# Performance work log

Measured on AMD Instinct MI355X. Metric: run time of the kernel, lower is better.

Reference implementation:

```python
import jax, jax.numpy as jnp
import numpy as np

N_NODES = 30000
N_EDGES = 480000
N_GRAPHS = 128
CONV_PARAMS = [[32, 32], [32, 32], [64, 64], [64, 64], [128, 128], [128, 128]]
IN_FEAT = 5
NUM_CENTROID = 100
NUM_CLASS = 2
BN_EPS = 1e-5


def setup_inputs() -> dict:
    key = jax.random.key(0)
    ks = jax.random.split(key, 64)
    inp = {}
    inp['features'] = jax.random.normal(ks[0], (N_NODES, IN_FEAT), jnp.float32)
    inp['src'] = jax.random.randint(ks[1], (N_EDGES,), 0, N_NODES, jnp.int32)
    inp['dst'] = jax.random.randint(ks[2], (N_EDGES,), 0, N_NODES, jnp.int32)
    inp['graph_id'] = jnp.sort(jax.random.randint(ks[3], (N_NODES,), 0, N_GRAPHS, jnp.int32))
    inp['bn_gamma'] = jnp.ones((IN_FEAT,), jnp.float32)
    inp['bn_beta'] = jnp.zeros((IN_FEAT,), jnp.float32)
    in_f = IN_FEAT
    ki = 4
    for i, (c1, c2) in enumerate(CONV_PARAMS):
        # EdgeConv MLP operates on concat([x_i, x_j - x_i]) -> 2*in_f inputs
        s1 = 1.0 / np.sqrt(2 * in_f)
        s2 = 1.0 / np.sqrt(c1)
        inp[f'W1_{i}'] = jax.random.normal(ks[ki], (2 * in_f, c1), jnp.float32) * s1
        inp[f'b1_{i}'] = jnp.zeros((c1,), jnp.float32)
        inp[f'W2_{i}'] = jax.random.normal(ks[ki + 1], (c1, c2), jnp.float32) * s2
        inp[f'b2_{i}'] = jnp.zeros((c2,), jnp.float32)
        ki += 2
        in_f = c2
    inp['centroids'] = jax.random.normal(ks[ki], (NUM_CENTROID, CONV_PARAMS[-1][-1]), jnp.float32)
    inp['fc_w'] = jax.random.normal(ks[ki + 1], (NUM_CENTROID, NUM_CLASS), jnp.float32) * (1.0 / np.sqrt(NUM_CENTROID))
    inp['fc_b'] = jnp.zeros((NUM_CLASS,), jnp.float32)
    return inp


def _edge_conv(x, src, dst, deg_inv, W1, b1, W2, b2):
    # DGCNN-style EdgeConv: MLP([x_i, x_j - x_i]) then mean-aggregate to dst node
    xi = x[dst]                                   # [E, F]
    xj = x[src]                                   # [E, F]
    e = jnp.concatenate([xi, xj - xi], axis=-1)   # [E, 2F]
    h = jax.nn.relu(e @ W1 + b1)
    h = jax.nn.relu(h @ W2 + b2)
    return jax.ops.segment_sum(h, dst, num_segments=x.shape[0]) * deg_inv


def reference(features, src, dst, graph_id, bn_gamma, bn_beta,
              W1_0, b1_0, W2_0, b2_0, W1_1, b1_1, W2_1, b2_1,
              W1_2, b1_2, W2_2, b2_2, W1_3, b1_3, W2_3, b2_3,
              W1_4, b1_4, W2_4, b2_4, W1_5, b1_5, W2_5, b2_5,
              centroids, fc_w, fc_b):
    N = features.shape[0]
    # BatchNorm1d in training mode (batch statistics over nodes)
    mu = features.mean(axis=0)
    var = features.var(axis=0)
    x = (features - mu) / jnp.sqrt(var + BN_EPS) * bn_gamma + bn_beta

    # in-degree for mean aggregation
    deg = jax.ops.segment_sum(jnp.ones_like(dst, jnp.float32), dst, num_segments=N)
    deg_inv = (1.0 / jnp.maximum(deg, 1.0))[:, None]

    params = [(W1_0, b1_0, W2_0, b2_0), (W1_1, b1_1, W2_1, b2_1),
              (W1_2, b1_2, W2_2, b2_2), (W1_3, b1_3, W2_3, b2_3),
              (W1_4, b1_4, W2_4, b2_4), (W1_5, b1_5, W2_5, b2_5)]
    for W1, b1, W2, b2 in params:
        x = _edge_conv(x, src, dst, deg_inv, W1, b1, W2, b2)  # [N, c2]

    # CentroidDistance (Euclidean manifold): dist of each node to each centroid
    diff = x[:, None, :] - centroids[None, :, :]              # [N, C, D]
    dist = jnp.sqrt(jnp.sum(diff * diff, axis=-1) + 1e-12)    # [N, C]

    # per-graph mean pooling of centroid distances
    cnt = jax.ops.segment_sum(jnp.ones((N,), jnp.float32), graph_id, num_segments=N_GRAPHS)
    pooled = jax.ops.segment_sum(dist, graph_id, num_segments=N_GRAPHS) / jnp.maximum(cnt, 1.0)[:, None]

    return pooled @ fc_w + fc_b  # [G, num_class]
```

## Files before the change

kernel.cpp:

```cpp
#include <hip/hip_runtime.h>
#include <hip/hip_fp16.h>

#define N_NODES 30000
#define N_EDGES 480000
#define N_GRAPHS 128
#define IN_FEAT 5
#define NUM_CENTROID 100
#define BN_EPS 1e-5f

typedef unsigned int u32;
typedef unsigned short u16;

using half8 = __attribute__((ext_vector_type(8))) _Float16;
using h2    = __attribute__((ext_vector_type(2))) _Float16;
using f32x4 = __attribute__((ext_vector_type(4))) float;

__device__ __forceinline__ u16 f2h(float x) {
    return __half_as_ushort(__float2half_rn(x));
}
__device__ __forceinline__ float h2f(u16 h) {
    return __half2float(__ushort_as_half(h));
}
__device__ __forceinline__ u32 pack2h(float lo, float hi) {
    return (u32)f2h(lo) | ((u32)f2h(hi) << 16);
}

#define BN_BLKS 118
__global__ __launch_bounds__(256) void setup1_kernel(
    const float* __restrict__ f, float* __restrict__ acc,
    const int* __restrict__ dst, int* __restrict__ counts)
{
    __shared__ float s[10];
    const int b = blockIdx.x;
    if (b < BN_BLKS) {
        if (threadIdx.x < 10) s[threadIdx.x] = 0.f;
        __syncthreads();
        int n = b * 256 + threadIdx.x;
        if (n < N_NODES) {
            #pragma unroll
            for (int k = 0; k < IN_FEAT; ++k) {
                float v = f[n * IN_FEAT + k];
                atomicAdd(&s[k], v);
                atomicAdd(&s[5 + k], v * v);
            }
        }
        __syncthreads();
        if (threadIdx.x < 10) atomicAdd(&acc[threadIdx.x], s[threadIdx.x]);
    } else {
        int e = (b - BN_BLKS) * 256 + threadIdx.x;
        if (e < N_EDGES) atomicAdd(&counts[dst[e]], 1);
    }
}

__global__ __launch_bounds__(1024) void scan_kernel(
    const int* __restrict__ counts, int* __restrict__ row_off,
    float* __restrict__ deg_inv, int N)
{
    __shared__ int s[1024];
    const int CH = 30;
    int t = threadIdx.x;
    int base = t * CH;
    int loc = 0;
    for (int j = 0; j < CH; ++j) {
        int i = base + j;
        if (i < N) loc += counts[i];
    }
    s[t] = loc;
    __syncthreads();
    for (int off = 1; off < 1024; off <<= 1) {
        int v = (t >= off) ? s[t - off] : 0;
        __syncthreads();
        s[t] += v;
        __syncthreads();
    }
    int run = s[t] - loc;
    for (int j = 0; j < CH; ++j) {
        int i = base + j;
        if (i < N) {
            int cv = counts[i];
            row_off[i] = run;
            run += cv;
            deg_inv[i] = 1.0f / fmaxf((float)cv, 1.0f);
        }
    }
    if (t == 1023) row_off[N] = s[1023];
}

__constant__ __device__ const int LFIN[6] = {5, 32, 32, 64, 64, 128};
__constant__ __device__ const int LKD[6]  = {32, 32, 32, 64, 64, 128};
__constant__ __device__ const int LCD[6]  = {32, 32, 64, 64, 128, 128};
__constant__ __device__ const int W1OFF[6] = {0, 2048, 4096, 8192, 16384, 32768};
__constant__ __device__ const int W2OFF[6] = {0, 1024, 2048, 6144, 10240, 26624};
#define W1TOT 65536
#define W2TOT 43008
#define CTOT  14336
#define PREP_TOT (W1TOT + W2TOT + CTOT + 112)

#define CSR_BLKS 1875
#define BNN_BLKS 586

struct Setup2Args {
    const int* dst; const int* src; const int* row_off; int* cursor;
    int* csr_src; int* csr_dst;
    const float* f; const float* acc; const float* gamma; const float* beta;
    float* X0;
    const float* w1[6]; const float* w2[6]; const float* cent;
    u16* w1img; u16* w2img; u16* centimg; float* csq;
};

__global__ __launch_bounds__(256) void setup2_kernel(Setup2Args a)
{
    const int b = blockIdx.x;
    if (b < CSR_BLKS) {
        int e = b * 256 + threadIdx.x;
        if (e < N_EDGES) {
            int d = a.dst[e];
            int p = atomicAdd(&a.cursor[d], 1);
            a.csr_src[a.row_off[d] + p] = a.src[e];
            a.csr_dst[a.row_off[d] + p] = d;
        }
        return;
    }
    if (b < CSR_BLKS + BNN_BLKS) {
        int i = (b - CSR_BLKS) * 256 + threadIdx.x;
        if (i < N_NODES * IN_FEAT) {
            int k = i % IN_FEAT;
            float mu = a.acc[k] / (float)N_NODES;
            float var = a.acc[5 + k] / (float)N_NODES - mu * mu;
            float sc = a.gamma[k] / sqrtf(var + BN_EPS);
            a.X0[i] = (a.f[i] - mu) * sc + a.beta[k];
        }
        return;
    }
    int gid = (b - CSR_BLKS - BNN_BLKS) * 256 + threadIdx.x;
    if (gid < W1TOT) {
        int l = 0;
        #pragma unroll
        for (int i = 1; i < 6; ++i) if (gid >= W1OFF[i]) l = i;
        int local = gid - W1OFF[l];
        int K = LKD[l], C = LCD[l], F = LFIN[l];
        int n = local / K, k = local % K;
        float v = 0.f;
        if (k < F) {
            if (n < C) v = a.w1[l][k * C + n] - a.w1[l][(F + k) * C + n];
            else       v = a.w1[l][(F + k) * C + (n - C)];
        }
        int byte = (local * 2) ^ ((n & 7) << 4);
        *(u16*)((char*)a.w1img + (size_t)W1OFF[l] * 2 + byte) = f2h(v);
        return;
    }
    int g2 = gid - W1TOT;
    if (g2 < W2TOT) {
        int l = 0;
        #pragma unroll
        for (int i = 1; i < 6; ++i) if (g2 >= W2OFF[i]) l = i;
        int local = g2 - W2OFF[l];
        int C = LCD[l];
        int n = local / C, k = local % C;
        float v = a.w2[l][k * C + n];
        int byte = (local * 2) ^ ((n & 7) << 4);
        *(u16*)((char*)a.w2img + (size_t)W2OFF[l] * 2 + byte) = f2h(v);
        return;
    }
    int g3 = g2 - W2TOT;
    if (g3 < CTOT) {
        int c = g3 / 128, d = g3 % 128;
        float v = (c < NUM_CENTROID) ? a.cent[c * 128 + d] : 0.f;
        int byte = (g3 * 2) ^ ((c & 7) << 4);
        *(u16*)((char*)a.centimg + byte) = f2h(v);
        return;
    }
    int c = g3 - CTOT;
    if (c < 112) {
        float s = 0.f;
        if (c < NUM_CENTROID) {
            for (int d = 0; d < 128; ++d) {
                float cv = h2f(f2h(a.cent[c * 128 + d]));
                s += cv * cv;
            }
        }
        a.csq[c] = s;
    }
}

template <int FIN, int K, int C>
__global__ __launch_bounds__(256) void node_mfma_kernel(
    const float* __restrict__ Xin, const float* __restrict__ scale,
    const u16* __restrict__ w1img, const float* __restrict__ b1,
    u16* __restrict__ U, u16* __restrict__ V, int N)
{
    constexpr int COLS = 2 * C;
    __shared__ u16 wt[COLS * K];
    __shared__ u16 xt[32 * K];

    for (int i = threadIdx.x; i < COLS * K / 8; i += 256)
        reinterpret_cast<uint4*>(wt)[i] = reinterpret_cast<const uint4*>(w1img)[i];

    constexpr int DPT = K / 8;
    const int nl = threadIdx.x >> 3;
    const int part = threadIdx.x & 7;
    const int n = blockIdx.x * 32 + nl;
    const int k0 = part * DPT;
    const bool vld = (n < N);
    float s = 1.f;
    if (vld && scale) s = scale[n];

    float xv[DPT];
    if constexpr (FIN == K) {
        #pragma unroll
        for (int j4 = 0; j4 < DPT / 4; ++j4) {
            float4 f4 = {0, 0, 0, 0};
            if (vld) f4 = *reinterpret_cast<const float4*>(Xin + (size_t)n * FIN + k0 + j4 * 4);
            xv[j4 * 4 + 0] = f4.x * s; xv[j4 * 4 + 1] = f4.y * s;
            xv[j4 * 4 + 2] = f4.z * s; xv[j4 * 4 + 3] = f4.w * s;
        }
    } else {
        #pragma unroll
        for (int j = 0; j < DPT; ++j) {
            int k = k0 + j;
            xv[j] = (vld && k < FIN) ? Xin[(size_t)n * FIN + k] * s : 0.f;
        }
    }

    if constexpr (DPT == 4) {
        u32 o[2];
        o[0] = pack2h(xv[0], xv[1]);
        o[1] = pack2h(xv[2], xv[3]);
        int byte = ((nl * K + k0) * 2) ^ ((nl & 7) << 4);
        *reinterpret_cast<uint2*>((char*)xt + byte) = *reinterpret_cast<uint2*>(o);
    } else {
        #pragma unroll
        for (int j8 = 0; j8 < DPT / 8; ++j8) {
            u32 o[4];
            #pragma unroll
            for (int q = 0; q < 4; ++q)
                o[q] = pack2h(xv[j8 * 8 + q * 2], xv[j8 * 8 + q * 2 + 1]);
            int byte = ((nl * K + k0 + j8 * 8) * 2) ^ ((nl & 7) << 4);
            *reinterpret_cast<uint4*>((char*)xt + byte) = *reinterpret_cast<uint4*>(o);
        }
    }
    __syncthreads();

    constexpr int NT = COLS / 16;
    constexpr int NPW = NT / 4;
    constexpr int KS = K / 32;

    const int wid = threadIdx.x >> 6;
    const int lane = threadIdx.x & 63;
    const int lrow = lane & 15;
    const int lk8 = (lane >> 4) * 8;

    f32x4 acc[2][NPW] = {};

    #pragma unroll
    for (int ks = 0; ks < KS; ++ks) {
        half8 afrag[2];
        #pragma unroll
        for (int m = 0; m < 2; ++m) {
            int row = m * 16 + lrow;
            int byte = ((row * K + ks * 32 + lk8) * 2) ^ ((row & 7) << 4);
            afrag[m] = *reinterpret_cast<const half8*>((const char*)xt + byte);
        }
        #pragma unroll
        for (int nn = 0; nn < NPW; ++nn) {
            int colr = (wid * NPW + nn) * 16 + lrow;
            int byte = ((colr * K + ks * 32 + lk8) * 2) ^ ((colr & 7) << 4);
            half8 bfrag = *reinterpret_cast<const half8*>((const char*)wt + byte);
            #pragma unroll
            for (int m = 0; m < 2; ++m)
                acc[m][nn] = __builtin_amdgcn_mfma_f32_16x16x32_f16(
                    afrag[m], bfrag, acc[m][nn], 0, 0, 0);
        }
    }

    #pragma unroll
    for (int nn = 0; nn < NPW; ++nn) {
        int colr = (wid * NPW + nn) * 16 + lrow;
        float bias = (colr < C) ? b1[colr] : 0.f;
        #pragma unroll
        for (int m = 0; m < 2; ++m) {
            #pragma unroll
            for (int j = 0; j < 4; ++j) {
                int row = m * 16 + (lane >> 4) * 4 + j;
                int node = blockIdx.x * 32 + row;
                if (node < N) {
                    float z = acc[m][nn][j] + bias;
                    if (colr < C) U[(size_t)node * C + colr] = f2h(z);
                    else          V[(size_t)node * C + colr - C] = f2h(z);
                }
            }
        }
    }
}

template <int C, int ET>
__global__ __launch_bounds__(256, 4) void edge_agg_kernel(
    const u16* __restrict__ U, const u16* __restrict__ V,
    const int* __restrict__ csr_src, const int* __restrict__ csr_dst,
    const u16* __restrict__ w2img, const float* __restrict__ b2,
    float* __restrict__ Xout, int E)
{
    constexpr int PAD = 2;
    __shared__ u16 at[ET * (C + PAD)];
    __shared__ int dstid[ET];

    constexpr int MT = ET / 16;
    constexpr int NT = C / 16;
    constexpr int WN = (NT < 4) ? NT : 4;
    constexpr int WM = 4 / WN;
    constexpr int MPW = MT / WM;
    constexpr int NPW = NT / WN;
    constexpr int KS = C / 32;

    const int wid = threadIdx.x >> 6;
    const int lane = threadIdx.x & 63;
    const int wn = wid % WN;
    const int wm = wid / WN;
    const int lrow = lane & 15;
    const int lk8 = (lane >> 4) * 8;

    half8 bfrag[NPW][KS];
    #pragma unroll
    for (int n = 0; n < NPW; ++n) {
        int col = (wn * NPW + n) * 16 + lrow;
        #pragma unroll
        for (int ks = 0; ks < KS; ++ks) {
            int byte = ((col * C + ks * 32 + lk8) * 2) ^ ((col & 7) << 4);
            bfrag[n][ks] = *reinterpret_cast<const half8*>((const char*)w2img + byte);
        }
    }

    constexpr int TPE = 256 / ET;
    const int e_loc = threadIdx.x / TPE;
    const int part  = threadIdx.x % TPE;
    const int k0 = part * 32;
    const int e = blockIdx.x * ET + e_loc;
    const bool valid = (e < E);
    const int dn = valid ? csr_dst[e] : 0;
    const int sn = valid ? csr_src[e] : 0;
    if (part == 0) dstid[e_loc] = valid ? dn : -1;

    const h2 zz = {(_Float16)0.f, (_Float16)0.f};
    const u16* Ur = U + (size_t)dn * C + k0;
    const u16* Vr = V + (size_t)sn * C + k0;
    #pragma unroll
    for (int j = 0; j < 4; ++j) {
        uint4 uu = {0, 0, 0, 0}, vv = {0, 0, 0, 0};
        if (valid) {
            uu = *reinterpret_cast<const uint4*>(Ur + j * 8);
            vv = *reinterpret_cast<const uint4*>(Vr + j * 8);
        }
        h2 o[4];
        const h2* ua = reinterpret_cast<const h2*>(&uu);
        const h2* va = reinterpret_cast<const h2*>(&vv);
        #pragma unroll
        for (int q = 0; q < 4; ++q)
            o[q] = __builtin_elementwise_max(ua[q] + va[q], zz);
        int byte = ((e_loc * C + k0 + j * 8) * 2) ^ ((e_loc & 7) << 4);
        *reinterpret_cast<uint4*>((char*)at + byte) = *reinterpret_cast<const uint4*>(o);
    }
    __syncthreads();

    f32x4 acc[MPW][NPW] = {};

    #pragma unroll
    for (int ks = 0; ks < KS; ++ks) {
        half8 afrag[MPW];
        #pragma unroll
        for (int m = 0; m < MPW; ++m) {
            int row = (wm * MPW + m) * 16 + lrow;
            int byte = ((row * C + ks * 32 + lk8) * 2) ^ ((row & 7) << 4);
            afrag[m] = *reinterpret_cast<const half8*>((const char*)at + byte);
        }
        #pragma unroll
        for (int m = 0; m < MPW; ++m)
            #pragma unroll
            for (int n = 0; n < NPW; ++n)
                acc[m][n] = __builtin_amdgcn_mfma_f32_16x16x32_f16(
                    afrag[m], bfrag[n][ks], acc[m][n], 0, 0, 0);
    }
    __syncthreads();

    #pragma unroll
    for (int m = 0; m < MPW; ++m) {
        #pragma unroll
        for (int n = 0; n < NPW; ++n) {
            int col = (wn * NPW + n) * 16 + lrow;
            float bb = b2[col];
            #pragma unroll
            for (int j = 0; j < 4; ++j) {
                int row = (wm * MPW + m) * 16 + (lane >> 4) * 4 + j;
                at[row * (C + PAD) + col] = f2h(fmaxf(acc[m][n][j] + bb, 0.f));
            }
        }
    }
    __syncthreads();

    constexpr int EPS = ET * C / 256;
    const int col = threadIdx.x & (C - 1);
    const int e0 = (threadIdx.x / C) * EPS;
    float sum = 0.f;
    int cur = dstid[e0];
    #pragma unroll 4
    for (int ee = e0; ee < e0 + EPS; ++ee) {
        int d = dstid[ee];
        if (d != cur) {
            if (cur >= 0) atomicAdd(&Xout[(size_t)cur * C + col], sum);
            sum = 0.f;
            cur = d;
        }
        sum += h2f(at[ee * (C + PAD) + col]);
    }
    if (cur >= 0) atomicAdd(&Xout[(size_t)cur * C + col], sum);
}

__global__ __launch_bounds__(256) void dist_mfma_kernel(
    const float* __restrict__ X, const float* __restrict__ scale,
    const u16* __restrict__ centimg, const float* __restrict__ csq,
    float* __restrict__ dist, int N)
{
    __shared__ u16 ct[112 * 128];
    __shared__ u16 xt[64 * 128];
    __shared__ float xsqp[64][4];
    __shared__ float csqs[112];

    for (int i = threadIdx.x; i < 112 * 128 / 8; i += 256)
        reinterpret_cast<uint4*>(ct)[i] = reinterpret_cast<const uint4*>(centimg)[i];
    if (threadIdx.x < 112) csqs[threadIdx.x] = csq[threadIdx.x];

    const int nl = threadIdx.x >> 2;
    const int part = threadIdx.x & 3;
    const int n = blockIdx.x * 64 + nl;
    const int k0 = part * 32;
    const bool vld = (n < N);
    const float s = vld ? scale[n] : 0.f;

    float ss = 0.f;
    #pragma unroll
    for (int j8 = 0; j8 < 4; ++j8) {
        float4 f0 = {0, 0, 0, 0}, f1 = {0, 0, 0, 0};
        if (vld) {
            f0 = *reinterpret_cast<const float4*>(X + (size_t)n * 128 + k0 + j8 * 8);
            f1 = *reinterpret_cast<const float4*>(X + (size_t)n * 128 + k0 + j8 * 8 + 4);
        }
        float xv[8] = {f0.x * s, f0.y * s, f0.z * s, f0.w * s,
                       f1.x * s, f1.y * s, f1.z * s, f1.w * s};
        u32 o[4];
        #pragma unroll
        for (int q = 0; q < 4; ++q) {
            float lo = h2f(f2h(xv[q * 2]));
            float hi = h2f(f2h(xv[q * 2 + 1]));
            ss += lo * lo + hi * hi;
            o[q] = pack2h(xv[q * 2], xv[q * 2 + 1]);
        }
        int byte = ((nl * 128 + k0 + j8 * 8) * 2) ^ ((nl & 7) << 4);
        *reinterpret_cast<uint4*>((char*)xt + byte) = *reinterpret_cast<uint4*>(o);
    }
    xsqp[nl][part] = ss;
    __syncthreads();

    const int wid = threadIdx.x >> 6;
    const int lane = threadIdx.x & 63;
    const int lrow = lane & 15;
    const int lk8 = (lane >> 4) * 8;

    f32x4 acc[7] = {};
    #pragma unroll
    for (int ks = 0; ks < 4; ++ks) {
        int row = wid * 16 + lrow;
        int byte = ((row * 128 + ks * 32 + lk8) * 2) ^ ((row & 7) << 4);
        half8 afrag = *reinterpret_cast<const half8*>((const char*)xt + byte);
        #pragma unroll
        for (int nn = 0; nn < 7; ++nn) {
            int colr = nn * 16 + lrow;
            int bb = ((colr * 128 + ks * 32 + lk8) * 2) ^ ((colr & 7) << 4);
            half8 bfrag = *reinterpret_cast<const half8*>((const char*)ct + bb);
            acc[nn] = __builtin_amdgcn_mfma_f32_16x16x32_f16(afrag, bfrag, acc[nn], 0, 0, 0);
        }
    }

    float xs[4];
    #pragma unroll
    for (int j = 0; j < 4; ++j) {
        int row = wid * 16 + (lane >> 4) * 4 + j;
        xs[j] = xsqp[row][0] + xsqp[row][1] + xsqp[row][2] + xsqp[row][3];
    }
    #pragma unroll
    for (int nn = 0; nn < 7; ++nn) {
        int colr = nn * 16 + lrow;
        if (colr < NUM_CENTROID) {
            float cq = csqs[colr];
            #pragma unroll
            for (int j = 0; j < 4; ++j) {
                int row = wid * 16 + (lane >> 4) * 4 + j;
                int node = blockIdx.x * 64 + row;
                if (node < N) {
                    float v = xs[j] - 2.f * acc[nn][j] + cq;
                    dist[(size_t)node * NUM_CENTROID + colr] = sqrtf(fmaxf(v, 0.f) + 1e-12f);
                }
            }
        }
    }
}

__global__ __launch_bounds__(128) void pool_fc_kernel(
    const float* __restrict__ dist, const int* __restrict__ gid,
    const float* __restrict__ fc_w, const float* __restrict__ fc_b,
    float* __restrict__ out, int N)
{
    __shared__ float pooled[NUM_CENTROID];
    const int g = blockIdx.x;
    const int t = threadIdx.x;

    int lo = 0, hi = N;
    while (lo < hi) { int mid = (lo + hi) >> 1; if (gid[mid] < g) lo = mid + 1; else hi = mid; }
    const int start = lo;
    hi = N;
    while (lo < hi) { int mid = (lo + hi) >> 1; if (gid[mid] < g + 1) lo = mid + 1; else hi = mid; }
    const int end = lo;

    if (t < NUM_CENTROID) {
        float s = 0.f;
        for (int n = start; n < end; ++n) s += dist[(size_t)n * NUM_CENTROID + t];
        pooled[t] = s / fmaxf((float)(end - start), 1.0f);
    }
    __syncthreads();
    if (t < 2) {
        float o = fc_b[t];
        for (int c = 0; c < NUM_CENTROID; ++c) o += pooled[c] * fc_w[c * 2 + t];
        out[g * 2 + t] = o;
    }
}

static const int W1OFF_H[6] = {0, 2048, 4096, 8192, 16384, 32768};
static const int W2OFF_H[6] = {0, 1024, 2048, 6144, 10240, 26624};

extern "C" void kernel_launch(void* const* d_in, const int* in_sizes, int n_in,
                              void* d_out, int out_size, void* d_ws, size_t ws_size,
                              hipStream_t stream) {
    const float* features = (const float*)d_in[0];
    const int*   src      = (const int*)d_in[1];
    const int*   dst      = (const int*)d_in[2];
    const int*   gid      = (const int*)d_in[3];
    const float* gamma    = (const float*)d_in[4];
    const float* beta     = (const float*)d_in[5];
    const float *W1[6], *b1[6], *W2[6], *b2[6];
    for (int i = 0; i < 6; ++i) {
        W1[i] = (const float*)d_in[6 + 4 * i];
        b1[i] = (const float*)d_in[7 + 4 * i];
        W2[i] = (const float*)d_in[8 + 4 * i];
        b2[i] = (const float*)d_in[9 + 4 * i];
    }
    const float* centroids = (const float*)d_in[30];
    const float* fc_w      = (const float*)d_in[31];
    const float* fc_b      = (const float*)d_in[32];

    const int N = N_NODES, E = N_EDGES;

    char* p = (char*)d_ws;
    size_t off = 0;
    auto alloc = [&](size_t bytes) {
        void* r = p + off;
        off += (bytes + 255) & ~(size_t)255;
        return r;
    };

    float* X0bn = (float*)alloc((size_t)N * IN_FEAT * 4);
    char* xz0 = p + off;
    float* XL[6];
    const int LCC[6] = {32, 32, 64, 64, 128, 128};
    for (int i = 0; i < 6; ++i) XL[i] = (float*)alloc((size_t)N * LCC[i] * 4);
    size_t xzbytes = (size_t)((p + off) - xz0);

    u16* Uh = (u16*)alloc((size_t)N * 128 * 2);
    u16* Vh = (u16*)alloc((size_t)N * 128 * 2);
    float* distb = (float*)Uh;

    int*   row_off = (int*)alloc((size_t)(N + 1) * 4);
    int*   csr_src = (int*)alloc((size_t)E * 4);
    int*   csr_dst = (int*)alloc((size_t)E * 4);
    float* deg_inv = (float*)alloc((size_t)N * 4);
    u16*   w1img   = (u16*)alloc((size_t)W1TOT * 2);
    u16*   w2img   = (u16*)alloc((size_t)W2TOT * 2);
    u16*   centimg = (u16*)alloc((size_t)CTOT * 2);
    float* csq     = (float*)alloc(112 * 4);

    char*  zero0   = (char*)(p + off);
    int*   counts  = (int*)alloc((size_t)N * 4);
    int*   cursor  = (int*)alloc((size_t)N * 4);
    float* bnacc   = (float*)alloc(64);
    size_t zbytes  = (size_t)((char*)(p + off) - zero0);

    (void)hipMemsetAsync(xz0, 0, xzbytes, stream);
    (void)hipMemsetAsync(zero0, 0, zbytes, stream);

    setup1_kernel<<<BN_BLKS + 1875, 256, 0, stream>>>(features, bnacc, dst, counts);
    scan_kernel<<<1, 1024, 0, stream>>>(counts, row_off, deg_inv, N);

    Setup2Args sa;
    sa.dst = dst; sa.src = src; sa.row_off = row_off; sa.cursor = cursor;
    sa.csr_src = csr_src; sa.csr_dst = csr_dst;
    sa.f = features; sa.acc = bnacc; sa.gamma = gamma; sa.beta = beta; sa.X0 = X0bn;
    for (int i = 0; i < 6; ++i) { sa.w1[i] = W1[i]; sa.w2[i] = W2[i]; }
    sa.cent = centroids; sa.w1img = w1img; sa.w2img = w2img;
    sa.centimg = centimg; sa.csq = csq;
    const int S2B = CSR_BLKS + BNN_BLKS + (PREP_TOT + 255) / 256;
    setup2_kernel<<<S2B, 256, 0, stream>>>(sa);

    const int NB = (N + 31) / 32;

    node_mfma_kernel<5, 32, 32><<<NB, 256, 0, stream>>>(
        X0bn, (const float*)nullptr, w1img + W1OFF_H[0], b1[0], Uh, Vh, N);
    edge_agg_kernel<32, 256><<<(E + 255) / 256, 256, 0, stream>>>(
        Uh, Vh, csr_src, csr_dst, w2img + W2OFF_H[0], b2[0], XL[0], E);

    node_mfma_kernel<32, 32, 32><<<NB, 256, 0, stream>>>(
        XL[0], deg_inv, w1img + W1OFF_H[1], b1[1], Uh, Vh, N);
    edge_agg_kernel<32, 256><<<(E + 255) / 256, 256, 0, stream>>>(
        Uh, Vh, csr_src, csr_dst, w2img + W2OFF_H[1], b2[1], XL[1], E);

    node_mfma_kernel<32, 32, 64><<<NB, 256, 0, stream>>>(
        XL[1], deg_inv, w1img + W1OFF_H[2], b1[2], Uh, Vh, N);
    edge_agg_kernel<64, 128><<<(E + 127) / 128, 256, 0, stream>>>(
        Uh, Vh, csr_src, csr_dst, w2img + W2OFF_H[2], b2[2], XL[2], E);

    node_mfma_kernel<64, 64, 64><<<NB, 256, 0, stream>>>(
        XL[2], deg_inv, w1img + W1OFF_H[3], b1[3], Uh, Vh, N);
    edge_agg_kernel<64, 128><<<(E + 127) / 128, 256, 0, stream>>>(
        Uh, Vh, csr_src, csr_dst, w2img + W2OFF_H[3], b2[3], XL[3], E);

    node_mfma_kernel<64, 64, 128><<<NB, 256, 0, stream>>>(
        XL[3], deg_inv, w1img + W1OFF_H[4], b1[4], Uh, Vh, N);
    edge_agg_kernel<128, 64><<<(E + 63) / 64, 256, 0, stream>>>(
        Uh, Vh, csr_src, csr_dst, w2img + W2OFF_H[4], b2[4], XL[4], E);

    node_mfma_kernel<128, 128, 128><<<NB, 256, 0, stream>>>(
        XL[4], deg_inv, w1img + W1OFF_H[5], b1[5], Uh, Vh, N);
    edge_agg_kernel<128, 64><<<(E + 63) / 64, 256, 0, stream>>>(
        Uh, Vh, csr_src, csr_dst, w2img + W2OFF_H[5], b2[5], XL[5], E);

    dist_mfma_kernel<<<(N + 63) / 64, 256, 0, stream>>>(XL[5], deg_inv, centimg, csq, distb, N);
    pool_fc_kernel<<<N_GRAPHS, 128, 0, stream>>>(distb, gid, fc_w, fc_b, (float*)d_out, N);
}
```

Measured before the change: 572.8 us.

## Fuse centroid distance with per-graph pooling via shared-memory segmented atomics

The distance kernel now writes its 64x100 distance tile to shared memory and, with graph ids staged in LDS, reduces it per graph before atomically adding partial sums into a small per-graph accumulator. This removes the full N x 100 distance write and re-read, and replaces the old pooling kernel, which ran only 128 blocks each scanning its graph serially. Per-graph node counts are now computed in the setup kernel, and a tiny one-block FC kernel divides by them and applies the linear layer. The cost is extra syncs and LDS reuse in the distance kernel, and float atomics that make summation order nondeterministic.

```diff
diff --git a/kernel.cpp b/kernel.cpp
--- a/kernel.cpp
+++ b/kernel.cpp
@@ -26,9 +26,11 @@
 }
 
 #define BN_BLKS 118
+#define DSTH_BLKS 1875
 __global__ __launch_bounds__(256) void setup1_kernel(
     const float* __restrict__ f, float* __restrict__ acc,
-    const int* __restrict__ dst, int* __restrict__ counts)
+    const int* __restrict__ dst, int* __restrict__ counts,
+    const int* __restrict__ gid, int* __restrict__ gcnt)
 {
     __shared__ float s[10];
     const int b = blockIdx.x;
@@ -46,9 +48,12 @@
         }
         __syncthreads();
         if (threadIdx.x < 10) atomicAdd(&acc[threadIdx.x], s[threadIdx.x]);
-    } else {
+    } else if (b < BN_BLKS + DSTH_BLKS) {
         int e = (b - BN_BLKS) * 256 + threadIdx.x;
         if (e < N_EDGES) atomicAdd(&counts[dst[e]], 1);
+    } else {
+        int n = (b - BN_BLKS - DSTH_BLKS) * 256 + threadIdx.x;
+        if (n < N_NODES) atomicAdd(&gcnt[gid[n]], 1);
     }
 }
 
@@ -414,19 +419,26 @@
     if (cur >= 0) atomicAdd(&Xout[(size_t)cur * C + col], sum);
 }
 
-__global__ __launch_bounds__(256) void dist_mfma_kernel(
+__global__ __launch_bounds__(256) void dist_pool_kernel(
     const float* __restrict__ X, const float* __restrict__ scale,
     const u16* __restrict__ centimg, const float* __restrict__ csq,
-    float* __restrict__ dist, int N)
+    const int* __restrict__ gid, float* __restrict__ psum, int N)
 {
-    __shared__ u16 ct[112 * 128];
-    __shared__ u16 xt[64 * 128];
-    __shared__ float xsqp[64][4];
-    __shared__ float csqs[112];
+    __shared__ char smem[46784];
+    u16* ct = (u16*)smem;
+    u16* xt = (u16*)(smem + 28672);
+    float* xsqp = (float*)(smem + 45056);
+    float* csqs = (float*)(smem + 46080);
+    int* gidS   = (int*)(smem + 46528);
+    float* dt   = (float*)smem;
 
     for (int i = threadIdx.x; i < 112 * 128 / 8; i += 256)
         reinterpret_cast<uint4*>(ct)[i] = reinterpret_cast<const uint4*>(centimg)[i];
     if (threadIdx.x < 112) csqs[threadIdx.x] = csq[threadIdx.x];
+    if (threadIdx.x < 64) {
+        int n = blockIdx.x * 64 + threadIdx.x;
+        gidS[threadIdx.x] = (n < N) ? gid[n] : -1;
+    }
 
     const int nl = threadIdx.x >> 2;
     const int part = threadIdx.x & 3;
@@ -456,7 +468,7 @@
         int byte = ((nl * 128 + k0 + j8 * 8) * 2) ^ ((nl & 7) << 4);
         *reinterpret_cast<uint4*>((char*)xt + byte) = *reinterpret_cast<uint4*>(o);
     }
-    xsqp[nl][part] = ss;
+    xsqp[nl * 4 + part] = ss;
     __syncthreads();
 
     const int wid = threadIdx.x >> 6;
@@ -483,53 +495,52 @@
     #pragma unroll
     for (int j = 0; j < 4; ++j) {
         int row = wid * 16 + (lane >> 4) * 4 + j;
-        xs[j] = xsqp[row][0] + xsqp[row][1] + xsqp[row][2] + xsqp[row][3];
-    }
+        xs[j] = xsqp[row * 4 + 0] + xsqp[row * 4 + 1] + xsqp[row * 4 + 2] + xsqp[row * 4 + 3];
+    }
+    __syncthreads();
+
     #pragma unroll
     for (int nn = 0; nn < 7; ++nn) {
         int colr = nn * 16 + lrow;
-        if (colr < NUM_CENTROID) {
-            float cq = csqs[colr];
-            #pragma unroll
-            for (int j = 0; j < 4; ++j) {
-                int row = wid * 16 + (lane >> 4) * 4 + j;
-                int node = blockIdx.x * 64 + row;
-                if (node < N) {
-                    float v = xs[j] - 2.f * acc[nn][j] + cq;
-                    dist[(size_t)node * NUM_CENTROID + colr] = sqrtf(fmaxf(v, 0.f) + 1e-12f);
-                }
+        float cq = csqs[colr];
+        #pragma unroll
+        for (int j = 0; j < 4; ++j) {
+            int row = wid * 16 + (lane >> 4) * 4 + j;
+            float v = xs[j] - 2.f * acc[nn][j] + cq;
+            dt[row * 112 + colr] = sqrtf(fmaxf(v, 0.f) + 1e-12f);
+        }
+    }
+    __syncthreads();
+
+    if (threadIdx.x < NUM_CENTROID) {
+        const int col = threadIdx.x;
+        float sum = 0.f;
+        int cur = gidS[0];
+        for (int r = 0; r < 64; ++r) {
+            int g = gidS[r];
+            if (g != cur) {
+                if (cur >= 0) atomicAdd(&psum[cur * NUM_CENTROID + col], sum);
+                sum = 0.f;
+                cur = g;
             }
-        }
-    }
-}
-
-__global__ __launch_bounds__(128) void pool_fc_kernel(
-    const float* __restrict__ dist, const int* __restrict__ gid,
+            if (g >= 0) sum += dt[r * 112 + col];
+        }
+        if (cur >= 0) atomicAdd(&psum[cur * NUM_CENTROID + col], sum);
+    }
+}
+
+__global__ __launch_bounds__(256) void fc_kernel(
+    const float* __restrict__ psum, const int* __restrict__ gcnt,
     const float* __restrict__ fc_w, const float* __restrict__ fc_b,
-    float* __restrict__ out, int N)
+    float* __restrict__ out)
 {
-    __shared__ float pooled[NUM_CENTROID];
-    const int g = blockIdx.x;
-    const int t = threadIdx.x;
-
-    int lo = 0, hi = N;
-    while (lo < hi) { int mid = (lo + hi) >> 1; if (gid[mid] < g) lo = mid + 1; else hi = mid; }
-    const int start = lo;
-    hi = N;
-    while (lo < hi) { int mid = (lo + hi) >> 1; if (gid[mid] < g + 1) lo = mid + 1; else hi = mid; }
-    const int end = lo;
-
-    if (t < NUM_CENTROID) {
-        float s = 0.f;
-        for (int n = start; n < end; ++n) s += dist[(size_t)n * NUM_CENTROID + t];
-        pooled[t] = s / fmaxf((float)(end - start), 1.0f);
-    }
-    __syncthreads();
-    if (t < 2) {
-        float o = fc_b[t];
-        for (int c = 0; c < NUM_CENTROID; ++c) o += pooled[c] * fc_w[c * 2 + t];
-        out[g * 2 + t] = o;
-    }
+    const int g = threadIdx.x >> 1;
+    const int cls = threadIdx.x & 1;
+    float o = 0.f;
+    for (int c = 0; c < NUM_CENTROID; ++c)
+        o += psum[g * NUM_CENTROID + c] * fc_w[c * 2 + cls];
+    float cnt = fmaxf((float)gcnt[g], 1.0f);
+    out[g * 2 + cls] = fc_b[cls] + o / cnt;
 }
 
 static const int W1OFF_H[6] = {0, 2048, 4096, 8192, 16384, 32768};
@@ -574,7 +585,6 @@
 
     u16* Uh = (u16*)alloc((size_t)N * 128 * 2);
     u16* Vh = (u16*)alloc((size_t)N * 128 * 2);
-    float* distb = (float*)Uh;
 
     int*   row_off = (int*)alloc((size_t)(N + 1) * 4);
     int*   csr_src = (int*)alloc((size_t)E * 4);
@@ -589,12 +599,15 @@
     int*   counts  = (int*)alloc((size_t)N * 4);
     int*   cursor  = (int*)alloc((size_t)N * 4);
     float* bnacc   = (float*)alloc(64);
+    float* psum    = (float*)alloc((size_t)N_GRAPHS * NUM_CENTROID * 4);
+    int*   gcnt    = (int*)alloc((size_t)N_GRAPHS * 4);
     size_t zbytes  = (size_t)((char*)(p + off) - zero0);
 
     (void)hipMemsetAsync(xz0, 0, xzbytes, stream);
     (void)hipMemsetAsync(zero0, 0, zbytes, stream);
 
-    setup1_kernel<<<BN_BLKS + 1875, 256, 0, stream>>>(features, bnacc, dst, counts);
+    setup1_kernel<<<BN_BLKS + DSTH_BLKS + BN_BLKS, 256, 0, stream>>>(
+        features, bnacc, dst, counts, gid, gcnt);
     scan_kernel<<<1, 1024, 0, stream>>>(counts, row_off, deg_inv, N);
 
     Setup2Args sa;
@@ -639,6 +652,7 @@
     edge_agg_kernel<128, 64><<<(E + 63) / 64, 256, 0, stream>>>(
         Uh, Vh, csr_src, csr_dst, w2img + W2OFF_H[5], b2[5], XL[5], E);
 
-    dist_mfma_kernel<<<(N + 63) / 64, 256, 0, stream>>>(XL[5], deg_inv, centimg, csq, distb, N);
-    pool_fc_kernel<<<N_GRAPHS, 128, 0, stream>>>(distb, gid, fc_w, fc_b, (float*)d_out, N);
-}
+    dist_pool_kernel<<<(N + 63) / 64, 256, 0, stream>>>(
+        XL[5], deg_inv, centimg, csq, gid, psum, N);
+    fc_kernel<<<1, 256, 0, stream>>>(psum, gcnt, fc_w, fc_b, (float*)d_out);
+}
```

Result: no change. 573.3 us (+0.1%).
